# Kernel optimization log

Measured on AMD Instinct MI355X. Metric: run time of the kernel, lower is better.

## Reference

```python
import jax, jax.numpy as jnp
import numpy as np

N, E, H, NH = 50000, 800000, 128, 4
D = H // NH
EPS = 1e-5


def _ln(x, g, b):
    m = jnp.mean(x, axis=-1, keepdims=True)
    v = jnp.mean((x - m) ** 2, axis=-1, keepdims=True)
    return (x - m) * jax.lax.rsqrt(v + EPS) * g + b


def setup_inputs() -> dict:
    key = jax.random.key(0)
    ks = jax.random.split(key, 16)

    def lin(k, fi, fo):
        w = jax.random.normal(k, (fi, fo), jnp.float32) * (1.0 / np.sqrt(fi))
        return w, jnp.zeros((fo,), jnp.float32)

    h = jax.random.normal(ks[0], (N, H), jnp.float32)
    e = jax.random.normal(ks[1], (E, H), jnp.float32)
    src = jax.random.randint(ks[2], (E,), 0, N, jnp.int32)
    dst = jax.random.randint(ks[3], (E,), 0, N, jnp.int32)

    Wq, bq = lin(ks[4], H, H)
    Wk, bk = lin(ks[5], 2 * H, H)
    Wv, bv = lin(ks[6], 2 * H, H)
    Wn1, bn1 = lin(ks[7], H, H)
    Wn2, bn2 = lin(ks[8], H, H)
    We1, be1 = lin(ks[9], 3 * H, H)
    We2, be2 = lin(ks[10], H, H)
    gh = jnp.ones((H,), jnp.float32)
    bh = jnp.zeros((H,), jnp.float32)
    ge = jnp.ones((H,), jnp.float32)
    be = jnp.zeros((H,), jnp.float32)

    return dict(h=h, e=e, src=src, dst=dst, Wq=Wq, bq=bq, Wk=Wk, bk=bk,
                Wv=Wv, bv=bv, Wn1=Wn1, bn1=bn1, Wn2=Wn2, bn2=bn2,
                We1=We1, be1=be1, We2=We2, be2=be2, gh=gh, bh=bh, ge=ge, be=be)


def reference(h, e, src, dst, Wq, bq, Wk, bk, Wv, bv, Wn1, bn1, Wn2, bn2,
              We1, be1, We2, be2, gh, bh, ge, be):
    # gather src node features onto edges, concat with edge features: [E, 2H]
    m = jnp.concatenate([h[src], e], axis=-1)
    Q = (h @ Wq + bq).reshape(N, NH, D)
    K = (m @ Wk + bk).reshape(E, NH, D)
    V = (m @ Wv + bv).reshape(E, NH, D)

    # per-edge multihead attention score against destination query: [E, NH]
    s = jnp.sum(Q[dst] * K, axis=-1) / np.sqrt(D).astype(np.float32)

    # destination-grouped (segment) softmax per head
    smax = jax.ops.segment_max(s, dst, num_segments=N)  # [N, NH]
    a = jnp.exp(s - smax[dst])
    denom = jax.ops.segment_sum(a, dst, num_segments=N)  # [N, NH]
    a = a / denom[dst]

    # weighted scatter-sum of values back to destination nodes
    msg = V * a[..., None]  # [E, NH, D]
    h_agg = jax.ops.segment_sum(msg, dst, num_segments=N).reshape(N, H)

    # node MLP update (dropout = identity in eval) + residual + LayerNorm
    h_new = jax.nn.relu(jax.nn.relu(h_agg @ Wn1 + bn1) @ Wn2 + bn2)
    h_out = _ln(h + h_new, gh, bh)

    # edge MLP update on [src_h, dst_h, e] + residual + LayerNorm
    me = jnp.concatenate([h_out[src], h_out[dst], e], axis=-1)  # [E, 3H]
    e_new = jax.nn.relu(jax.nn.relu(me @ We1 + be1) @ We2 + be2)
    e_out = _ln(e + e_new, ge, be)
    return h_out, e_out
```

## Files before the change

### kernel.cpp

```cpp
#include <hip/hip_runtime.h>
#include <hip/hip_bf16.h>

#define NN 50000
#define EE 800000
#define HH 128

typedef __attribute__((ext_vector_type(8))) short bf16x8;
typedef __attribute__((ext_vector_type(4))) float f32x4;

__device__ inline unsigned short f2bf(float f) {
    union { float f; unsigned u; } v; v.f = f;
    unsigned r = v.u + 0x7FFF + ((v.u >> 16) & 1);
    return (unsigned short)(r >> 16);
}

__global__ __launch_bounds__(256) void hist_k(const int* __restrict__ dst, int* __restrict__ cnt) {
    int i = blockIdx.x * 256 + threadIdx.x;
    if (i < EE) atomicAdd(&cnt[dst[i]], 1);
}

__global__ __launch_bounds__(256) void blocksum_k(const int* __restrict__ cnt, int* __restrict__ bsum) {
    __shared__ int sm[256];
    int i = blockIdx.x * 256 + threadIdx.x;
    sm[threadIdx.x] = (i < NN) ? cnt[i] : 0;
    __syncthreads();
    for (int s = 128; s > 0; s >>= 1) {
        if (threadIdx.x < s) sm[threadIdx.x] += sm[threadIdx.x + s];
        __syncthreads();
    }
    if (threadIdx.x == 0) bsum[blockIdx.x] = sm[0];
}

__global__ __launch_bounds__(256) void scanb_k(int* __restrict__ bsum, int nb) {
    __shared__ int sm[256];
    int t = threadIdx.x;
    sm[t] = (t < nb) ? bsum[t] : 0;
    __syncthreads();
    for (int d = 1; d < 256; d <<= 1) {
        int v = (t >= d) ? sm[t - d] : 0;
        __syncthreads();
        sm[t] += v;
        __syncthreads();
    }
    if (t < nb) bsum[t] = sm[t];
}

__global__ __launch_bounds__(256) void offsets_k(const int* __restrict__ cnt, const int* __restrict__ bsum,
                                                 int* __restrict__ offsets, int* __restrict__ cursor) {
    __shared__ int sm[256];
    int b = blockIdx.x, t = threadIdx.x;
    int i = b * 256 + t;
    int c = (i < NN) ? cnt[i] : 0;
    sm[t] = c;
    __syncthreads();
    for (int d = 1; d < 256; d <<= 1) {
        int v = (t >= d) ? sm[t - d] : 0;
        __syncthreads();
        sm[t] += v;
        __syncthreads();
    }
    int incl = sm[t];
    int base = (b == 0) ? 0 : bsum[b - 1];
    int off = base + incl - c;
    if (i < NN) { offsets[i] = off; cursor[i] = off; }
    if (i == NN - 1) offsets[NN] = off + c;
}

__global__ __launch_bounds__(256) void fill_k(const int* __restrict__ src, const int* __restrict__ dst,
                                              int* __restrict__ cursor, int* __restrict__ eids,
                                              int* __restrict__ srcc, int* __restrict__ dstc) {
    int i = blockIdx.x * 256 + threadIdx.x;
    if (i < EE) {
        int d = dst[i];
        int p = atomicAdd(&cursor[d], 1);
        eids[p] = i;
        srcc[p] = src[i];
        dstc[p] = d;
    }
}

__global__ __launch_bounds__(256) void wprep_k(const float* __restrict__ W, unsigned short* __restrict__ out,
                                               int fi, int fo, int n_off, int out_ld) {
    int i = blockIdx.x * 256 + threadIdx.x;
    if (i >= fi * fo) return;
    int n = i / fi, k = i - n * fi;
    out[(size_t)(n_off + n) * out_ld + k] = f2bf(W[(size_t)k * fo + n]);
}

__global__ __launch_bounds__(256) void cvt_k(const float* __restrict__ in, unsigned short* __restrict__ out,
                                             long n8) {
    long i = (long)blockIdx.x * 256 + threadIdx.x;
    if (i >= n8) return;
    const float4* p = (const float4*)in + i * 2;
    float4 a = p[0], b = p[1];
    bf16x8 o = {(short)f2bf(a.x), (short)f2bf(a.y), (short)f2bf(a.z), (short)f2bf(a.w),
                (short)f2bf(b.x), (short)f2bf(b.y), (short)f2bf(b.z), (short)f2bf(b.w)};
    *((bf16x8*)out + i) = o;
}

__global__ __launch_bounds__(256) void cvtcsr_k(const float* __restrict__ e, const int* __restrict__ eids,
                                                unsigned short* __restrict__ out) {
    long gid = (long)blockIdx.x * 256 + threadIdx.x;
    long j = gid >> 4;
    if (j >= EE) return;
    int part = (int)(gid & 15);
    int rid = eids[j];
    const float4* p = (const float4*)(e + (size_t)rid * HH + part * 8);
    float4 a = p[0], b = p[1];
    bf16x8 o = {(short)f2bf(a.x), (short)f2bf(a.y), (short)f2bf(a.z), (short)f2bf(a.w),
                (short)f2bf(b.x), (short)f2bf(b.y), (short)f2bf(b.z), (short)f2bf(b.w)};
    *((bf16x8*)(out + (size_t)j * HH + part * 8)) = o;
}

template <int G, int NCW, int RT, int MODE>
__global__ __launch_bounds__(512, 2) void mm4_k(
    const unsigned short* __restrict__ A0, const int* __restrict__ idx0,
    const unsigned short* __restrict__ Wt, const float* __restrict__ bias,
    int M,
    float* __restrict__ Cf, unsigned short* __restrict__ Cb, int out_ld)
{
    constexpr int RW = 8 / NCW;
    constexpr int ROWS = RW * RT * 16;
    constexpr int Ktot = G * 128;
    constexpr int SI = ROWS / 32;
    __shared__ unsigned short Asl[G * ROWS * 128];

    const int t = threadIdx.x;
    const int wid = t >> 6, lane = t & 63;
    const int lr = lane & 15, lk = lane >> 4;
    const int colw = wid & 3;
    const int roww = wid >> 2;
    const int col0 = colw << 5;
    const int tbase = blockIdx.x * ROWS;

    #pragma unroll
    for (int g = 0; g < G; ++g) {
        #pragma unroll
        for (int i = 0; i < SI; ++i) {
            int rl = ((i * 8 + wid) << 2) + (lane >> 4);
            int gr = tbase + rl; if (gr >= M) gr = M - 1;
            int rid = idx0 ? idx0[gr] : gr;
            const unsigned short* src = A0 + (size_t)rid * HH + (((lane & 15) ^ (rl & 7)) << 3);
            unsigned short* dst = &Asl[(g * ROWS + ((i * 8 + wid) << 2)) << 7];
            __builtin_amdgcn_global_load_lds((const __attribute__((address_space(1))) void*)src,
                                             (__attribute__((address_space(3))) void*)dst, 16, 0, 0);
        }
    }

    f32x4 acc[RT][2];
    #pragma unroll
    for (int tt = 0; tt < RT; ++tt) { acc[tt][0] = (f32x4){0,0,0,0}; acc[tt][1] = (f32x4){0,0,0,0}; }

    __syncthreads();

    #pragma unroll
    for (int g = 0; g < G; ++g) {
        bf16x8 b[4][2];
        #pragma unroll
        for (int s = 0; s < 4; ++s)
            #pragma unroll
            for (int c = 0; c < 2; ++c)
                b[s][c] = *(const bf16x8*)(Wt + (size_t)(col0 + (c << 4) + lr) * Ktot + (g << 7) + (s << 5) + (lk << 3));

        #pragma unroll
        for (int tt = 0; tt < RT; ++tt) {
            const int tl = (tt * RW + roww) << 4;
            bf16x8 a[4];
            #pragma unroll
            for (int s = 0; s < 4; ++s) {
                const int c16 = ((s << 2) + lk) ^ (lr & 7);
                a[s] = *(const bf16x8*)&Asl[((g * ROWS + tl + lr) << 7) + (c16 << 3)];
            }
            #pragma unroll
            for (int s = 0; s < 4; ++s) {
                acc[tt][0] = __builtin_amdgcn_mfma_f32_16x16x32_bf16(a[s], b[s][0], acc[tt][0], 0, 0, 0);
                acc[tt][1] = __builtin_amdgcn_mfma_f32_16x16x32_bf16(a[s], b[s][1], acc[tt][1], 0, 0, 0);
            }
        }
    }

    float bias2[2] = {bias[col0 + lr], bias[col0 + 16 + lr]};
    #pragma unroll
    for (int tt = 0; tt < RT; ++tt) {
        #pragma unroll
        for (int rr = 0; rr < 4; ++rr) {
            int row = tbase + ((tt * RW + roww) << 4) + (lk << 2) + rr;
            if (row >= M) continue;
            #pragma unroll
            for (int c = 0; c < 2; ++c) {
                float v = acc[tt][c][rr] + bias2[c];
                if (MODE == 1) v = fmaxf(v, 0.f);
                size_t o = (size_t)row * out_ld + col0 + (c << 4) + lr;
                if (MODE == 0 || MODE == 1) Cf[o] = v;
                else Cb[o] = f2bf(v);
            }
        }
    }
}

template <int G, int RT>
__global__ __launch_bounds__(512, 2) void mlp_k(
    const unsigned short* __restrict__ A0, const int* __restrict__ idx0,
    const unsigned short* __restrict__ W1t, const float* __restrict__ b1,
    const unsigned short* __restrict__ W2t, const float* __restrict__ b2,
    int M,
    float* __restrict__ Cf, unsigned short* __restrict__ Cb2,
    const float* __restrict__ resid, const float* __restrict__ gamma, const float* __restrict__ beta)
{
    constexpr int RW = 2, NCW = 4;
    constexpr int ROWS = RW * RT * 16;
    constexpr int K1 = G * 128;
    constexpr int SI = ROWS / 32;
    __shared__ unsigned short Asl[G * ROWS * 128];
    __shared__ float lnbuf[RT * 32 * 8];

    const int t = threadIdx.x;
    const int wid = t >> 6, lane = t & 63;
    const int lr = lane & 15, lk = lane >> 4;
    const int colw = wid & 3, roww = wid >> 2;
    const int col0 = colw << 5;
    const int tbase = blockIdx.x * ROWS;

    #pragma unroll
    for (int g = 0; g < G; ++g) {
        #pragma unroll
        for (int i = 0; i < SI; ++i) {
            int rl = ((i * 8 + wid) << 2) + (lane >> 4);
            int gr = tbase + rl; if (gr >= M) gr = M - 1;
            int rid = idx0 ? idx0[gr] : gr;
            const unsigned short* src = A0 + (size_t)rid * HH + (((lane & 15) ^ (rl & 7)) << 3);
            unsigned short* dst = &Asl[(g * ROWS + ((i * 8 + wid) << 2)) << 7];
            __builtin_amdgcn_global_load_lds((const __attribute__((address_space(1))) void*)src,
                                             (__attribute__((address_space(3))) void*)dst, 16, 0, 0);
        }
    }

    f32x4 acc[RT][2];
    #pragma unroll
    for (int tt = 0; tt < RT; ++tt) { acc[tt][0] = (f32x4){0,0,0,0}; acc[tt][1] = (f32x4){0,0,0,0}; }

    __syncthreads();

    #pragma unroll
    for (int g = 0; g < G; ++g) {
        bf16x8 b[4][2];
        #pragma unroll
        for (int s = 0; s < 4; ++s)
            #pragma unroll
            for (int c = 0; c < 2; ++c)
                b[s][c] = *(const bf16x8*)(W1t + (size_t)(col0 + (c << 4) + lr) * K1 + (g << 7) + (s << 5) + (lk << 3));

        #pragma unroll
        for (int tt = 0; tt < RT; ++tt) {
            const int tl = (tt * RW + roww) << 4;
            bf16x8 a[4];
            #pragma unroll
            for (int s = 0; s < 4; ++s) {
                const int c16 = ((s << 2) + lk) ^ (lr & 7);
                a[s] = *(const bf16x8*)&Asl[((g * ROWS + tl + lr) << 7) + (c16 << 3)];
            }
            #pragma unroll
            for (int s = 0; s < 4; ++s) {
                acc[tt][0] = __builtin_amdgcn_mfma_f32_16x16x32_bf16(a[s], b[s][0], acc[tt][0], 0, 0, 0);
                acc[tt][1] = __builtin_amdgcn_mfma_f32_16x16x32_bf16(a[s], b[s][1], acc[tt][1], 0, 0, 0);
            }
        }
    }

    __syncthreads();

    {
        float b1c[2] = {b1[col0 + lr], b1[col0 + 16 + lr]};
        #pragma unroll
        for (int tt = 0; tt < RT; ++tt) {
            #pragma unroll
            for (int rr = 0; rr < 4; ++rr) {
                int rowl = ((tt * RW + roww) << 4) + (lk << 2) + rr;
                #pragma unroll
                for (int c = 0; c < 2; ++c) {
                    int col = col0 + (c << 4) + lr;
                    int chunk = (col >> 3) ^ (rowl & 7);
                    Asl[(rowl << 7) + (chunk << 3) + (col & 7)] =
                        f2bf(fmaxf(acc[tt][c][rr] + b1c[c], 0.f));
                }
            }
        }
    }

    __syncthreads();

    f32x4 acc2[RT][2];
    #pragma unroll
    for (int tt = 0; tt < RT; ++tt) { acc2[tt][0] = (f32x4){0,0,0,0}; acc2[tt][1] = (f32x4){0,0,0,0}; }

    {
        bf16x8 b[4][2];
        #pragma unroll
        for (int s = 0; s < 4; ++s)
            #pragma unroll
            for (int c = 0; c < 2; ++c)
                b[s][c] = *(const bf16x8*)(W2t + (size_t)(col0 + (c << 4) + lr) * 128 + (s << 5) + (lk << 3));

        #pragma unroll
        for (int tt = 0; tt < RT; ++tt) {
            const int tl = (tt * RW + roww) << 4;
            bf16x8 a[4];
            #pragma unroll
            for (int s = 0; s < 4; ++s) {
                const int c16 = ((s << 2) + lk) ^ (lr & 7);
                a[s] = *(const bf16x8*)&Asl[((tl + lr) << 7) + (c16 << 3)];
            }
            #pragma unroll
            for (int s = 0; s < 4; ++s) {
                acc2[tt][0] = __builtin_amdgcn_mfma_f32_16x16x32_bf16(a[s], b[s][0], acc2[tt][0], 0, 0, 0);
                acc2[tt][1] = __builtin_amdgcn_mfma_f32_16x16x32_bf16(a[s], b[s][1], acc2[tt][1], 0, 0, 0);
            }
        }
    }

    float b2c[2] = {b2[col0 + lr], b2[col0 + 16 + lr]};
    float g2[2] = {gamma[col0 + lr], gamma[col0 + 16 + lr]};
    float be2[2] = {beta[col0 + lr], beta[col0 + 16 + lr]};

    #pragma unroll
    for (int tt = 0; tt < RT; ++tt) {
        #pragma unroll
        for (int rr = 0; rr < 4; ++rr) {
            int row = tbase + ((tt * RW + roww) << 4) + (lk << 2) + rr;
            int rowc = (row < M) ? row : M - 1;
            float sum = 0.f, sq = 0.f;
            #pragma unroll
            for (int c = 0; c < 2; ++c) {
                float v = fmaxf(acc2[tt][c][rr] + b2c[c], 0.f);
                v += resid[(size_t)rowc * HH + col0 + (c << 4) + lr];
                acc2[tt][c][rr] = v;
                sum += v; sq += v * v;
            }
            sum += __shfl_xor(sum, 1); sq += __shfl_xor(sq, 1);
            sum += __shfl_xor(sum, 2); sq += __shfl_xor(sq, 2);
            sum += __shfl_xor(sum, 4); sq += __shfl_xor(sq, 4);
            sum += __shfl_xor(sum, 8); sq += __shfl_xor(sq, 8);
            if (lr == 0) {
                int rls = (roww << 4) + (lk << 2) + rr;
                lnbuf[((tt * 32 + rls) << 3) + (colw << 1) + 0] = sum;
                lnbuf[((tt * 32 + rls) << 3) + (colw << 1) + 1] = sq;
            }
        }
    }
    __syncthreads();
    #pragma unroll
    for (int tt = 0; tt < RT; ++tt) {
        #pragma unroll
        for (int rr = 0; rr < 4; ++rr) {
            int rls = (roww << 4) + (lk << 2) + rr;
            float s4 = 0.f, q4 = 0.f;
            #pragma unroll
            for (int cw = 0; cw < 4; ++cw) {
                s4 += lnbuf[((tt * 32 + rls) << 3) + (cw << 1) + 0];
                q4 += lnbuf[((tt * 32 + rls) << 3) + (cw << 1) + 1];
            }
            const float mean = s4 * (1.f / 128.f);
            const float var = q4 * (1.f / 128.f) - mean * mean;
            const float rs = rsqrtf(var + 1e-5f);
            int row = tbase + ((tt * RW + roww) << 4) + (lk << 2) + rr;
            if (row < M) {
                #pragma unroll
                for (int c = 0; c < 2; ++c) {
                    float o = (acc2[tt][c][rr] - mean) * rs * g2[c] + be2[c];
                    size_t idx = (size_t)row * HH + col0 + (c << 4) + lr;
                    Cf[idx] = o;
                    if (Cb2) Cb2[idx] = f2bf(o);
                }
            }
        }
    }
}

__global__ __launch_bounds__(512, 2) void mlpe_k(
    const unsigned short* __restrict__ ho, const int* __restrict__ src,
    const int* __restrict__ dst, const float* __restrict__ e,
    const unsigned short* __restrict__ W1t, const float* __restrict__ b1,
    const unsigned short* __restrict__ W2t, const float* __restrict__ b2,
    int M,
    float* __restrict__ Cf,
    const float* __restrict__ gamma, const float* __restrict__ beta)
{
    constexpr int RW = 2, RT = 2;
    constexpr int ROWS = RW * RT * 16;
    constexpr int K1 = 384;
    __shared__ unsigned short Asl[2 * ROWS * 128];
    __shared__ float Esl[ROWS * 128];
    __shared__ float lnbuf[RT * 32 * 8];

    const int t = threadIdx.x;
    const int wid = t >> 6, lane = t & 63;
    const int lr = lane & 15, lk = lane >> 4;
    const int colw = wid & 3, roww = wid >> 2;
    const int col0 = colw << 5;
    const int tbase = blockIdx.x * ROWS;

    #pragma unroll
    for (int g = 0; g < 2; ++g) {
        const int* ig = g ? dst : src;
        #pragma unroll
        for (int i = 0; i < 2; ++i) {
            int rl = ((i * 8 + wid) << 2) + (lane >> 4);
            int gr = tbase + rl; if (gr >= M) gr = M - 1;
            int rid = ig[gr];
            const unsigned short* sp = ho + (size_t)rid * HH + (((lane & 15) ^ (rl & 7)) << 3);
            unsigned short* dp = &Asl[(g * ROWS + ((i * 8 + wid) << 2)) << 7];
            __builtin_amdgcn_global_load_lds((const __attribute__((address_space(1))) void*)sp,
                                             (__attribute__((address_space(3))) void*)dp, 16, 0, 0);
        }
    }
    #pragma unroll
    for (int i = 0; i < 4; ++i) {
        int row = i * 16 + wid * 2 + (lane >> 5);
        int c16 = lane & 31;
        int c16s = (c16 & 24) | ((c16 & 7) ^ (row & 7));
        int gr = tbase + row; if (gr >= M) gr = M - 1;
        const float* sp = e + (size_t)gr * HH + c16s * 4;
        float* dp = &Esl[(i * 16 + wid * 2) * 128 + (lane >> 5) * 128];
        dp = &Esl[(i * 512 + wid * 64) * 4 / 4] + 0;
        float* dbase = Esl + (size_t)(i * 512 + wid * 64) * 4;
        (void)dp;
        __builtin_amdgcn_global_load_lds((const __attribute__((address_space(1))) void*)sp,
                                         (__attribute__((address_space(3))) void*)dbase, 16, 0, 0);
    }

    f32x4 acc[RT][2];
    #pragma unroll
    for (int tt = 0; tt < RT; ++tt) { acc[tt][0] = (f32x4){0,0,0,0}; acc[tt][1] = (f32x4){0,0,0,0}; }

    __syncthreads();

    #pragma unroll
    for (int g = 0; g < 3; ++g) {
        bf16x8 b[4][2];
        #pragma unroll
        for (int s = 0; s < 4; ++s)
            #pragma unroll
            for (int c = 0; c < 2; ++c)
                b[s][c] = *(const bf16x8*)(W1t + (size_t)(col0 + (c << 4) + lr) * K1 + (g << 7) + (s << 5) + (lk << 3));

        #pragma unroll
        for (int tt = 0; tt < RT; ++tt) {
            const int tl = (tt * RW + roww) << 4;
            const int r = tl + lr;
            bf16x8 a[4];
            if (g < 2) {
                #pragma unroll
                for (int s = 0; s < 4; ++s) {
                    const int c16 = ((s << 2) + lk) ^ (lr & 7);
                    a[s] = *(const bf16x8*)&Asl[((g * ROWS + r) << 7) + (c16 << 3)];
                }
            } else {
                #pragma unroll
                for (int s = 0; s < 4; ++s) {
                    int c16a = (s << 3) + (lk << 1);
                    int c16b = c16a + 1;
                    int ca = (c16a & 24) | ((c16a & 7) ^ (r & 7));
                    int cb = (c16b & 24) | ((c16b & 7) ^ (r & 7));
                    float4 fa = *(const float4*)&Esl[r * 128 + ca * 4];
                    float4 fb = *(const float4*)&Esl[r * 128 + cb * 4];
                    a[s] = (bf16x8){(short)f2bf(fa.x), (short)f2bf(fa.y), (short)f2bf(fa.z), (short)f2bf(fa.w),
                                    (short)f2bf(fb.x), (short)f2bf(fb.y), (short)f2bf(fb.z), (short)f2bf(fb.w)};
                }
            }
            #pragma unroll
            for (int s = 0; s < 4; ++s) {
                acc[tt][0] = __builtin_amdgcn_mfma_f32_16x16x32_bf16(a[s], b[s][0], acc[tt][0], 0, 0, 0);
                acc[tt][1] = __builtin_amdgcn_mfma_f32_16x16x32_bf16(a[s], b[s][1], acc[tt][1], 0, 0, 0);
            }
        }
    }

    __syncthreads();

    {
        float b1c[2] = {b1[col0 + lr], b1[col0 + 16 + lr]};
        #pragma unroll
        for (int tt = 0; tt < RT; ++tt) {
            #pragma unroll
            for (int rr = 0; rr < 4; ++rr) {
                int rowl = ((tt * RW + roww) << 4) + (lk << 2) + rr;
                #pragma unroll
                for (int c = 0; c < 2; ++c) {
                    int col = col0 + (c << 4) + lr;
                    int chunk = (col >> 3) ^ (rowl & 7);
                    Asl[(rowl << 7) + (chunk << 3) + (col & 7)] =
                        f2bf(fmaxf(acc[tt][c][rr] + b1c[c], 0.f));
                }
            }
        }
    }

    __syncthreads();

    f32x4 acc2[RT][2];
    #pragma unroll
    for (int tt = 0; tt < RT; ++tt) { acc2[tt][0] = (f32x4){0,0,0,0}; acc2[tt][1] = (f32x4){0,0,0,0}; }

    {
        bf16x8 b[4][2];
        #pragma unroll
        for (int s = 0; s < 4; ++s)
            #pragma unroll
            for (int c = 0; c < 2; ++c)
                b[s][c] = *(const bf16x8*)(W2t + (size_t)(col0 + (c << 4) + lr) * 128 + (s << 5) + (lk << 3));

        #pragma unroll
        for (int tt = 0; tt < RT; ++tt) {
            const int tl = (tt * RW + roww) << 4;
            bf16x8 a[4];
            #pragma unroll
            for (int s = 0; s < 4; ++s) {
                const int c16 = ((s << 2) + lk) ^ (lr & 7);
                a[s] = *(const bf16x8*)&Asl[((tl + lr) << 7) + (c16 << 3)];
            }
            #pragma unroll
            for (int s = 0; s < 4; ++s) {
                acc2[tt][0] = __builtin_amdgcn_mfma_f32_16x16x32_bf16(a[s], b[s][0], acc2[tt][0], 0, 0, 0);
                acc2[tt][1] = __builtin_amdgcn_mfma_f32_16x16x32_bf16(a[s], b[s][1], acc2[tt][1], 0, 0, 0);
            }
        }
    }

    float b2c[2] = {b2[col0 + lr], b2[col0 + 16 + lr]};
    float g2[2] = {gamma[col0 + lr], gamma[col0 + 16 + lr]};
    float be2[2] = {beta[col0 + lr], beta[col0 + 16 + lr]};

    #pragma unroll
    for (int tt = 0; tt < RT; ++tt) {
        #pragma unroll
        for (int rr = 0; rr < 4; ++rr) {
            int rowl = ((tt * RW + roww) << 4) + (lk << 2) + rr;
            float sum = 0.f, sq = 0.f;
            #pragma unroll
            for (int c = 0; c < 2; ++c) {
                int col = col0 + (c << 4) + lr;
                int c16 = col >> 2;
                int cs = (c16 & 24) | ((c16 & 7) ^ (rowl & 7));
                float rv = Esl[rowl * 128 + cs * 4 + (col & 3)];
                float v = fmaxf(acc2[tt][c][rr] + b2c[c], 0.f) + rv;
                acc2[tt][c][rr] = v;
                sum += v; sq += v * v;
            }
            sum += __shfl_xor(sum, 1); sq += __shfl_xor(sq, 1);
            sum += __shfl_xor(sum, 2); sq += __shfl_xor(sq, 2);
            sum += __shfl_xor(sum, 4); sq += __shfl_xor(sq, 4);
            sum += __shfl_xor(sum, 8); sq += __shfl_xor(sq, 8);
            if (lr == 0) {
                int rls = (roww << 4) + (lk << 2) + rr;
                lnbuf[((tt * 32 + rls) << 3) + (colw << 1) + 0] = sum;
                lnbuf[((tt * 32 + rls) << 3) + (colw << 1) + 1] = sq;
            }
        }
    }
    __syncthreads();
    #pragma unroll
    for (int tt = 0; tt < RT; ++tt) {
        #pragma unroll
        for (int rr = 0; rr < 4; ++rr) {
            int rls = (roww << 4) + (lk << 2) + rr;
            float s4 = 0.f, q4 = 0.f;
            #pragma unroll
            for (int cw = 0; cw < 4; ++cw) {
                s4 += lnbuf[((tt * 32 + rls) << 3) + (cw << 1) + 0];
                q4 += lnbuf[((tt * 32 + rls) << 3) + (cw << 1) + 1];
            }
            const float mean = s4 * (1.f / 128.f);
            const float var = q4 * (1.f / 128.f) - mean * mean;
            const float rs = rsqrtf(var + 1e-5f);
            int row = tbase + ((tt * RW + roww) << 4) + (lk << 2) + rr;
            if (row < M) {
                #pragma unroll
                for (int c = 0; c < 2; ++c)
                    Cf[(size_t)row * HH + col0 + (c << 4) + lr] =
                        (acc2[tt][c][rr] - mean) * rs * g2[c] + be2[c];
            }
        }
    }
}

template <int RT>
__global__ __launch_bounds__(512, 2) void kv_k(
    const unsigned short* __restrict__ hbf, const int* __restrict__ srcc,
    const unsigned short* __restrict__ ebfc,
    const unsigned short* __restrict__ Wt, const float* __restrict__ bias,
    const float* __restrict__ Q, const int* __restrict__ dstc,
    int M, unsigned short* __restrict__ V, float* __restrict__ sbuf)
{
    constexpr int ROWS = RT * 16;
    constexpr int Ktot = 256;
    constexpr int SI = ROWS / 32;
    __shared__ unsigned short Asl[2 * ROWS * 128];

    const int t = threadIdx.x;
    const int wid = t >> 6, lane = t & 63;
    const int lr = lane & 15, lk = lane >> 4;
    const int col0 = wid << 5;
    const int tbase = blockIdx.x * ROWS;

    int dstid[RT][4];
    if (wid < 4) {
        #pragma unroll
        for (int tt = 0; tt < RT; ++tt)
            #pragma unroll
            for (int rr = 0; rr < 4; ++rr) {
                int row = tbase + (tt << 4) + (lk << 2) + rr;
                dstid[tt][rr] = dstc[(row < M) ? row : M - 1];
            }
    }

    #pragma unroll
    for (int g = 0; g < 2; ++g) {
        const unsigned short* Ag = g ? ebfc : hbf;
        #pragma unroll
        for (int i = 0; i < SI; ++i) {
            int rl = ((i * 8 + wid) << 2) + (lane >> 4);
            int gr = tbase + rl; if (gr >= M) gr = M - 1;
            int rid = g ? gr : srcc[gr];
            const unsigned short* srcp = Ag + (size_t)rid * HH + (((lane & 15) ^ (rl & 7)) << 3);
            unsigned short* dstp = &Asl[(g * ROWS + ((i * 8 + wid) << 2)) << 7];
            __builtin_amdgcn_global_load_lds((const __attribute__((address_space(1))) void*)srcp,
                                             (__attribute__((address_space(3))) void*)dstp, 16, 0, 0);
        }
    }

    f32x4 acc[RT][2];
    #pragma unroll
    for (int tt = 0; tt < RT; ++tt) { acc[tt][0] = (f32x4){0,0,0,0}; acc[tt][1] = (f32x4){0,0,0,0}; }

    __syncthreads();

    #pragma unroll
    for (int g = 0; g < 2; ++g) {
        bf16x8 b[4][2];
        #pragma unroll
        for (int s = 0; s < 4; ++s)
            #pragma unroll
            for (int c = 0; c < 2; ++c)
                b[s][c] = *(const bf16x8*)(Wt + (size_t)(col0 + (c << 4) + lr) * Ktot + (g << 7) + (s << 5) + (lk << 3));

        #pragma unroll
        for (int tt = 0; tt < RT; ++tt) {
            bf16x8 a[4];
            #pragma unroll
            for (int s = 0; s < 4; ++s) {
                const int c16 = ((s << 2) + lk) ^ (lr & 7);
                a[s] = *(const bf16x8*)&Asl[((g * ROWS + (tt << 4) + lr) << 7) + (c16 << 3)];
            }
            #pragma unroll
            for (int s = 0; s < 4; ++s) {
                acc[tt][0] = __builtin_amdgcn_mfma_f32_16x16x32_bf16(a[s], b[s][0], acc[tt][0], 0, 0, 0);
                acc[tt][1] = __builtin_amdgcn_mfma_f32_16x16x32_bf16(a[s], b[s][1], acc[tt][1], 0, 0, 0);
            }
        }
    }

    float bias2[2] = {bias[col0 + lr], bias[col0 + 16 + lr]};

    if (wid < 4) {
        #pragma unroll
        for (int tt = 0; tt < RT; ++tt) {
            #pragma unroll
            for (int rr = 0; rr < 4; ++rr) {
                int row = tbase + (tt << 4) + (lk << 2) + rr;
                int d = dstid[tt][rr];
                float q0 = Q[(size_t)d * HH + col0 + lr];
                float q1 = Q[(size_t)d * HH + col0 + 16 + lr];
                float p = (acc[tt][0][rr] + bias2[0]) * q0 + (acc[tt][1][rr] + bias2[1]) * q1;
                p += __shfl_xor(p, 1); p += __shfl_xor(p, 2);
                p += __shfl_xor(p, 4); p += __shfl_xor(p, 8);
                if (lr == 0 && row < M)
                    sbuf[(size_t)row * 4 + wid] = p * 0.17677669529663687f;
            }
        }
    } else {
        #pragma unroll
        for (int tt = 0; tt < RT; ++tt) {
            #pragma unroll
            for (int rr = 0; rr < 4; ++rr) {
                int row = tbase + (tt << 4) + (lk << 2) + rr;
                if (row >= M) continue;
                #pragma unroll
                for (int c = 0; c < 2; ++c)
                    V[(size_t)row * HH + (col0 - 128) + (c << 4) + lr] = f2bf(acc[tt][c][rr] + bias2[c]);
            }
        }
    }
}

__global__ __launch_bounds__(256) void agg_k(const __hip_bfloat16* __restrict__ Vb,
                                             const float* __restrict__ s,
                                             const int* __restrict__ offsets,
                                             unsigned short* __restrict__ hagg)
{
    const int t = threadIdx.x;
    const int n = blockIdx.x * 4 + (t >> 6);
    if (n >= NN) return;
    const int lane = t & 63;
    const int c0 = lane, c1 = lane + 64;
    const int h0 = lane >> 5, h1 = h0 + 2;
    const int o0 = offsets[n], o1 = offsets[n + 1];
    float m0 = -1e30f, m1 = -1e30f, d0 = 0.f, d1 = 0.f, a0 = 0.f, a1 = 0.f;
    for (int j = o0; j < o1; ++j) {
        const float s0 = s[(size_t)j * 4 + h0];
        const float s1 = s[(size_t)j * 4 + h1];
        const float v0 = __bfloat162float(Vb[(size_t)j * HH + c0]);
        const float v1 = __bfloat162float(Vb[(size_t)j * HH + c1]);
        float nm = fmaxf(m0, s0);
        float sc = __expf(m0 - nm);
        float w  = __expf(s0 - nm);
        d0 = d0 * sc + w; a0 = a0 * sc + w * v0; m0 = nm;
        nm = fmaxf(m1, s1);
        sc = __expf(m1 - nm);
        w  = __expf(s1 - nm);
        d1 = d1 * sc + w; a1 = a1 * sc + w * v1; m1 = nm;
    }
    const bool any = (o1 > o0);
    hagg[(size_t)n * HH + c0] = any ? f2bf(a0 / d0) : 0;
    hagg[(size_t)n * HH + c1] = any ? f2bf(a1 / d1) : 0;
}

extern "C" void kernel_launch(void* const* d_in, const int* in_sizes, int n_in,
                              void* d_out, int out_size, void* d_ws, size_t ws_size,
                              hipStream_t stream)
{
    const float* h   = (const float*)d_in[0];
    const float* e   = (const float*)d_in[1];
    const int*   src = (const int*)d_in[2];
    const int*   dst = (const int*)d_in[3];
    const float* Wq  = (const float*)d_in[4];
    const float* bq  = (const float*)d_in[5];
    const float* Wk  = (const float*)d_in[6];
    const float* bk  = (const float*)d_in[7];
    const float* Wv  = (const float*)d_in[8];
    const float* bv  = (const float*)d_in[9];
    const float* Wn1 = (const float*)d_in[10];
    const float* bn1 = (const float*)d_in[11];
    const float* Wn2 = (const float*)d_in[12];
    const float* bn2 = (const float*)d_in[13];
    const float* We1 = (const float*)d_in[14];
    const float* be1 = (const float*)d_in[15];
    const float* We2 = (const float*)d_in[16];
    const float* be2 = (const float*)d_in[17];
    const float* gh  = (const float*)d_in[18];
    const float* bh  = (const float*)d_in[19];
    const float* ge  = (const float*)d_in[20];
    const float* be_ = (const float*)d_in[21];
    (void)in_sizes; (void)n_in; (void)out_size; (void)ws_size;

    float* h_out = (float*)d_out;
    float* e_out = (float*)d_out + (size_t)NN * HH;

    char* ws = (char*)d_ws;
    size_t off = 0;
    auto carve = [&](size_t bytes) { void* p = ws + off; off += (bytes + 255) & ~(size_t)255; return p; };
    unsigned short* Vbuf = (unsigned short*)carve((size_t)EE * HH * 2);
    unsigned short* ebfc = (unsigned short*)carve((size_t)EE * HH * 2);
    float* Q      = (float*)carve((size_t)NN * HH * 4);
    float* sbuf   = (float*)carve((size_t)EE * 4 * 4);
    unsigned short* hagg = (unsigned short*)carve((size_t)NN * HH * 2);
    unsigned short* hobf = (unsigned short*)carve((size_t)NN * HH * 2);
    unsigned short* hbf  = (unsigned short*)carve((size_t)NN * HH * 2);
    int* cursor   = (int*)carve((size_t)NN * 4);
    int* offsets  = (int*)carve((size_t)(NN + 1) * 4);
    int* bsum     = (int*)carve(256 * 4);
    int* eids     = (int*)carve((size_t)EE * 4);
    int* srcc     = (int*)carve((size_t)EE * 4);
    int* dstc     = (int*)carve((size_t)EE * 4);
    unsigned short* Wq_s  = (unsigned short*)carve(128 * 128 * 2);
    unsigned short* Wkv_s = (unsigned short*)carve(256 * 256 * 2);
    unsigned short* Wn1_s = (unsigned short*)carve(128 * 128 * 2);
    unsigned short* Wn2_s = (unsigned short*)carve(128 * 128 * 2);
    unsigned short* We1_s = (unsigned short*)carve(128 * 384 * 2);
    unsigned short* We2_s = (unsigned short*)carve(128 * 128 * 2);
    float* b_kv   = (float*)carve(256 * 4);

    const int nb = (NN + 255) / 256;

    wprep_k<<<(128 * 128 + 255) / 256, 256, 0, stream>>>(Wq,  Wq_s,  128, 128, 0, 128);
    wprep_k<<<(256 * 128 + 255) / 256, 256, 0, stream>>>(Wk,  Wkv_s, 256, 128, 0, 256);
    wprep_k<<<(256 * 128 + 255) / 256, 256, 0, stream>>>(Wv,  Wkv_s, 256, 128, 128, 256);
    wprep_k<<<(128 * 128 + 255) / 256, 256, 0, stream>>>(Wn1, Wn1_s, 128, 128, 0, 128);
    wprep_k<<<(128 * 128 + 255) / 256, 256, 0, stream>>>(Wn2, Wn2_s, 128, 128, 0, 128);
    wprep_k<<<(384 * 128 + 255) / 256, 256, 0, stream>>>(We1, We1_s, 384, 128, 0, 384);
    wprep_k<<<(128 * 128 + 255) / 256, 256, 0, stream>>>(We2, We2_s, 128, 128, 0, 128);
    hipMemcpyAsync(b_kv,       bk, 128 * 4, hipMemcpyDeviceToDevice, stream);
    hipMemcpyAsync(b_kv + 128, bv, 128 * 4, hipMemcpyDeviceToDevice, stream);

    cvt_k<<<(NN * HH / 8 + 255) / 256, 256, 0, stream>>>(h, hbf, (long)NN * HH / 8);

    hipMemsetAsync(cursor, 0, (size_t)NN * 4, stream);
    hist_k<<<(EE + 255) / 256, 256, 0, stream>>>(dst, cursor);
    blocksum_k<<<nb, 256, 0, stream>>>(cursor, bsum);
    scanb_k<<<1, 256, 0, stream>>>(bsum, nb);
    offsets_k<<<nb, 256, 0, stream>>>(cursor, bsum, offsets, cursor);
    fill_k<<<(EE + 255) / 256, 256, 0, stream>>>(src, dst, cursor, eids, srcc, dstc);

    cvtcsr_k<<<(EE * 16 + 255) / 256, 256, 0, stream>>>(e, eids, ebfc);

    mm4_k<1, 4, 4, 0><<<(NN + 127) / 128, 512, 0, stream>>>(
        hbf, nullptr, Wq_s, bq, NN, Q, nullptr, 128);

    kv_k<4><<<EE / 64, 512, 0, stream>>>(
        hbf, srcc, ebfc, Wkv_s, b_kv, Q, dstc, EE, Vbuf, sbuf);

    agg_k<<<(NN + 3) / 4, 256, 0, stream>>>((const __hip_bfloat16*)Vbuf, sbuf, offsets, hagg);

    mlp_k<1, 4><<<(NN + 127) / 128, 512, 0, stream>>>(
        hagg, nullptr, Wn1_s, bn1, Wn2_s, bn2, NN, h_out, hobf, h, gh, bh);

    mlpe_k<<<EE / 64, 512, 0, stream>>>(
        hobf, src, dst, e, We1_s, be1, We2_s, be2, EE, e_out, ge, be_);
}
```

Baseline: 1.246 ms.

## Make edge GEMM kernels persistent with double-buffered LDS staging

Both per-edge kernels (K/V projection with score, and the edge MLP with LayerNorm) become persistent: 500 blocks each loop over many tiles, with the next tile's gathered inputs loaded asynchronously into a second LDS buffer while the current tile is computed. The edge MLP tile shrinks to 32 rows, uses a separate buffer for the hidden activations, and uses a lighter LDS-only barrier between its stages. The aim is to hide gather latency and cut per-block launch and prologue overhead. In exchange LDS use per block grows, the grid is fixed at 500 blocks, which may leave CUs underused or unbalanced, and weights are still reloaded every tile.

```diff
diff --git a/kernel.cpp b/kernel.cpp
--- a/kernel.cpp
+++ b/kernel.cpp
@@ -12,6 +12,12 @@
     union { float f; unsigned u; } v; v.f = f;
     unsigned r = v.u + 0x7FFF + ((v.u >> 16) & 1);
     return (unsigned short)(r >> 16);
+}
+
+__device__ __forceinline__ void lds_barrier() {
+    asm volatile("s_waitcnt lgkmcnt(0)" ::: "memory");
+    __builtin_amdgcn_sched_barrier(0);
+    __builtin_amdgcn_s_barrier();
 }
 
 __global__ __launch_bounds__(256) void hist_k(const int* __restrict__ dst, int* __restrict__ cnt) {
@@ -376,7 +382,125 @@
     }
 }
 
-__global__ __launch_bounds__(512, 2) void mlpe_k(
+template <int TPB>
+__global__ __launch_bounds__(512, 2) void kvt_k(
+    const unsigned short* __restrict__ hbf, const int* __restrict__ srcc,
+    const unsigned short* __restrict__ ebfc,
+    const unsigned short* __restrict__ Wt, const float* __restrict__ bias,
+    const float* __restrict__ Q, const int* __restrict__ dstc,
+    int M, unsigned short* __restrict__ V, float* __restrict__ sbuf)
+{
+    __shared__ unsigned short Abuf[2][2 * 64 * 128];
+
+    const int t = threadIdx.x;
+    const int wid = t >> 6, lane = t & 63;
+    const int lr = lane & 15, lk = lane >> 4;
+    const int col0 = wid << 5;
+    const int tb = blockIdx.x * TPB;
+
+    auto stage = [&](int tile, int buf) {
+        const int base = tile * 64;
+        #pragma unroll
+        for (int g = 0; g < 2; ++g) {
+            const unsigned short* Ag = g ? ebfc : hbf;
+            #pragma unroll
+            for (int i = 0; i < 2; ++i) {
+                int rl = ((i * 8 + wid) << 2) + (lane >> 4);
+                int gr = base + rl; if (gr >= M) gr = M - 1;
+                int rid = g ? gr : srcc[gr];
+                const unsigned short* sp = Ag + (size_t)rid * HH + (((lane & 15) ^ (rl & 7)) << 3);
+                unsigned short* dp = &Abuf[buf][(g * 64 + ((i * 8 + wid) << 2)) << 7];
+                __builtin_amdgcn_global_load_lds((const __attribute__((address_space(1))) void*)sp,
+                                                 (__attribute__((address_space(3))) void*)dp, 16, 0, 0);
+            }
+        }
+    };
+
+    float bias2[2] = {bias[col0 + lr], bias[col0 + 16 + lr]};
+
+    stage(tb, 0);
+
+    for (int tt = 0; tt < TPB; ++tt) {
+        const int cur = tt & 1;
+        const int rbase = (tb + tt) * 64;
+
+        __syncthreads();
+        if (tt + 1 < TPB) stage(tb + tt + 1, cur ^ 1);
+
+        int dstid[4][4];
+        if (wid < 4) {
+            #pragma unroll
+            for (int t4 = 0; t4 < 4; ++t4)
+                #pragma unroll
+                for (int rr = 0; rr < 4; ++rr) {
+                    int row = rbase + (t4 << 4) + (lk << 2) + rr;
+                    dstid[t4][rr] = dstc[(row < M) ? row : M - 1];
+                }
+        }
+
+        f32x4 acc[4][2];
+        #pragma unroll
+        for (int t4 = 0; t4 < 4; ++t4) { acc[t4][0] = (f32x4){0,0,0,0}; acc[t4][1] = (f32x4){0,0,0,0}; }
+
+        #pragma unroll
+        for (int g = 0; g < 2; ++g) {
+            bf16x8 b[4][2];
+            #pragma unroll
+            for (int s = 0; s < 4; ++s)
+                #pragma unroll
+                for (int c = 0; c < 2; ++c)
+                    b[s][c] = *(const bf16x8*)(Wt + (size_t)(col0 + (c << 4) + lr) * 256 + (g << 7) + (s << 5) + (lk << 3));
+
+            #pragma unroll
+            for (int t4 = 0; t4 < 4; ++t4) {
+                bf16x8 a[4];
+                #pragma unroll
+                for (int s = 0; s < 4; ++s) {
+                    const int c16 = ((s << 2) + lk) ^ (lr & 7);
+                    a[s] = *(const bf16x8*)&Abuf[cur][((g * 64 + (t4 << 4) + lr) << 7) + (c16 << 3)];
+                }
+                #pragma unroll
+                for (int s = 0; s < 4; ++s) {
+                    acc[t4][0] = __builtin_amdgcn_mfma_f32_16x16x32_bf16(a[s], b[s][0], acc[t4][0], 0, 0, 0);
+                    acc[t4][1] = __builtin_amdgcn_mfma_f32_16x16x32_bf16(a[s], b[s][1], acc[t4][1], 0, 0, 0);
+                }
+            }
+        }
+
+        if (wid < 4) {
+            #pragma unroll
+            for (int t4 = 0; t4 < 4; ++t4) {
+                #pragma unroll
+                for (int rr = 0; rr < 4; ++rr) {
+                    int row = rbase + (t4 << 4) + (lk << 2) + rr;
+                    int d = dstid[t4][rr];
+                    float q0 = Q[(size_t)d * HH + col0 + lr];
+                    float q1 = Q[(size_t)d * HH + col0 + 16 + lr];
+                    float p = (acc[t4][0][rr] + bias2[0]) * q0 + (acc[t4][1][rr] + bias2[1]) * q1;
+                    p += __shfl_xor(p, 1); p += __shfl_xor(p, 2);
+                    p += __shfl_xor(p, 4); p += __shfl_xor(p, 8);
+                    if (lr == 0 && row < M)
+                        sbuf[(size_t)row * 4 + wid] = p * 0.17677669529663687f;
+                }
+            }
+        } else {
+            #pragma unroll
+            for (int t4 = 0; t4 < 4; ++t4) {
+                #pragma unroll
+                for (int rr = 0; rr < 4; ++rr) {
+                    int row = rbase + (t4 << 4) + (lk << 2) + rr;
+                    if (row >= M) continue;
+                    #pragma unroll
+                    for (int c = 0; c < 2; ++c)
+                        V[(size_t)row * HH + (col0 - 128) + (c << 4) + lr] = f2bf(acc[t4][c][rr] + bias2[c]);
+                }
+            }
+        }
+    }
+}
+
+template <int TPB>
+__global__ __launch_bounds__(512, 2) void mlpet_k(
     const unsigned short* __restrict__ ho, const int* __restrict__ src,
     const int* __restrict__ dst, const float* __restrict__ e,
     const unsigned short* __restrict__ W1t, const float* __restrict__ b1,
@@ -385,74 +509,74 @@
     float* __restrict__ Cf,
     const float* __restrict__ gamma, const float* __restrict__ beta)
 {
-    constexpr int RW = 2, RT = 2;
-    constexpr int ROWS = RW * RT * 16;
-    constexpr int K1 = 384;
-    __shared__ unsigned short Asl[2 * ROWS * 128];
-    __shared__ float Esl[ROWS * 128];
-    __shared__ float lnbuf[RT * 32 * 8];
+    __shared__ unsigned short Abuf[2][2 * 32 * 128];
+    __shared__ float Ebuf[2][32 * 128];
+    __shared__ unsigned short tbuf[32 * 128];
+    __shared__ float lnbuf[32 * 8];
 
     const int t = threadIdx.x;
     const int wid = t >> 6, lane = t & 63;
     const int lr = lane & 15, lk = lane >> 4;
-    const int colw = wid & 3, roww = wid >> 2;
+    const int colw = wid & 3, rg = wid >> 2;
     const int col0 = colw << 5;
-    const int tbase = blockIdx.x * ROWS;
-
-    #pragma unroll
-    for (int g = 0; g < 2; ++g) {
-        const int* ig = g ? dst : src;
-        #pragma unroll
-        for (int i = 0; i < 2; ++i) {
-            int rl = ((i * 8 + wid) << 2) + (lane >> 4);
-            int gr = tbase + rl; if (gr >= M) gr = M - 1;
+    const int tb = blockIdx.x * TPB;
+
+    auto stage = [&](int tile, int buf) {
+        const int base = tile * 32;
+        #pragma unroll
+        for (int g = 0; g < 2; ++g) {
+            const int* ig = g ? dst : src;
+            int rl = t >> 4;
+            int gr = base + rl; if (gr >= M) gr = M - 1;
             int rid = ig[gr];
-            const unsigned short* sp = ho + (size_t)rid * HH + (((lane & 15) ^ (rl & 7)) << 3);
-            unsigned short* dp = &Asl[(g * ROWS + ((i * 8 + wid) << 2)) << 7];
+            const unsigned short* sp = ho + (size_t)rid * HH + (((t & 15) ^ (rl & 7)) << 3);
+            unsigned short* dp = &Abuf[buf][((g * 32) << 7) + (wid << 9)];
             __builtin_amdgcn_global_load_lds((const __attribute__((address_space(1))) void*)sp,
                                              (__attribute__((address_space(3))) void*)dp, 16, 0, 0);
         }
-    }
-    #pragma unroll
-    for (int i = 0; i < 4; ++i) {
-        int row = i * 16 + wid * 2 + (lane >> 5);
-        int c16 = lane & 31;
-        int c16s = (c16 & 24) | ((c16 & 7) ^ (row & 7));
-        int gr = tbase + row; if (gr >= M) gr = M - 1;
-        const float* sp = e + (size_t)gr * HH + c16s * 4;
-        float* dp = &Esl[(i * 16 + wid * 2) * 128 + (lane >> 5) * 128];
-        dp = &Esl[(i * 512 + wid * 64) * 4 / 4] + 0;
-        float* dbase = Esl + (size_t)(i * 512 + wid * 64) * 4;
-        (void)dp;
-        __builtin_amdgcn_global_load_lds((const __attribute__((address_space(1))) void*)sp,
-                                         (__attribute__((address_space(3))) void*)dbase, 16, 0, 0);
-    }
-
-    f32x4 acc[RT][2];
-    #pragma unroll
-    for (int tt = 0; tt < RT; ++tt) { acc[tt][0] = (f32x4){0,0,0,0}; acc[tt][1] = (f32x4){0,0,0,0}; }
-
-    __syncthreads();
-
-    #pragma unroll
-    for (int g = 0; g < 3; ++g) {
-        bf16x8 b[4][2];
-        #pragma unroll
-        for (int s = 0; s < 4; ++s)
-            #pragma unroll
-            for (int c = 0; c < 2; ++c)
-                b[s][c] = *(const bf16x8*)(W1t + (size_t)(col0 + (c << 4) + lr) * K1 + (g << 7) + (s << 5) + (lk << 3));
-
-        #pragma unroll
-        for (int tt = 0; tt < RT; ++tt) {
-            const int tl = (tt * RW + roww) << 4;
-            const int r = tl + lr;
+        #pragma unroll
+        for (int i = 0; i < 2; ++i) {
+            int row = i * 16 + (t >> 5);
+            int c16 = t & 31;
+            int c16s = (c16 & 24) | ((c16 & 7) ^ (row & 7));
+            int gr = base + row; if (gr >= M) gr = M - 1;
+            const float* sp = e + (size_t)gr * HH + c16s * 4;
+            float* dp = Ebuf[buf] + i * 2048 + wid * 256;
+            __builtin_amdgcn_global_load_lds((const __attribute__((address_space(1))) void*)sp,
+                                             (__attribute__((address_space(3))) void*)dp, 16, 0, 0);
+        }
+    };
+
+    float b1c[2] = {b1[col0 + lr], b1[col0 + 16 + lr]};
+    float b2c[2] = {b2[col0 + lr], b2[col0 + 16 + lr]};
+    float g2[2]  = {gamma[col0 + lr], gamma[col0 + 16 + lr]};
+    float be2[2] = {beta[col0 + lr], beta[col0 + 16 + lr]};
+
+    stage(tb, 0);
+
+    for (int tt = 0; tt < TPB; ++tt) {
+        const int cur = tt & 1;
+        const int rbase = (tb + tt) * 32;
+
+        __syncthreads();
+        if (tt + 1 < TPB) stage(tb + tt + 1, cur ^ 1);
+
+        f32x4 acc[2] = {(f32x4){0,0,0,0}, (f32x4){0,0,0,0}};
+        const int r = rg * 16 + lr;
+        #pragma unroll
+        for (int g = 0; g < 3; ++g) {
+            bf16x8 b[4][2];
+            #pragma unroll
+            for (int s = 0; s < 4; ++s)
+                #pragma unroll
+                for (int c = 0; c < 2; ++c)
+                    b[s][c] = *(const bf16x8*)(W1t + (size_t)(col0 + (c << 4) + lr) * 384 + (g << 7) + (s << 5) + (lk << 3));
             bf16x8 a[4];
             if (g < 2) {
                 #pragma unroll
                 for (int s = 0; s < 4; ++s) {
                     const int c16 = ((s << 2) + lk) ^ (lr & 7);
-                    a[s] = *(const bf16x8*)&Asl[((g * ROWS + r) << 7) + (c16 << 3)];
+                    a[s] = *(const bf16x8*)&Abuf[cur][((g * 32 + r) << 7) + (c16 << 3)];
                 }
             } else {
                 #pragma unroll
@@ -461,89 +585,66 @@
                     int c16b = c16a + 1;
                     int ca = (c16a & 24) | ((c16a & 7) ^ (r & 7));
                     int cb = (c16b & 24) | ((c16b & 7) ^ (r & 7));
-                    float4 fa = *(const float4*)&Esl[r * 128 + ca * 4];
-                    float4 fb = *(const float4*)&Esl[r * 128 + cb * 4];
+                    float4 fa = *(const float4*)&Ebuf[cur][r * 128 + ca * 4];
+                    float4 fb = *(const float4*)&Ebuf[cur][r * 128 + cb * 4];
                     a[s] = (bf16x8){(short)f2bf(fa.x), (short)f2bf(fa.y), (short)f2bf(fa.z), (short)f2bf(fa.w),
                                     (short)f2bf(fb.x), (short)f2bf(fb.y), (short)f2bf(fb.z), (short)f2bf(fb.w)};
                 }
             }
             #pragma unroll
             for (int s = 0; s < 4; ++s) {
-                acc[tt][0] = __builtin_amdgcn_mfma_f32_16x16x32_bf16(a[s], b[s][0], acc[tt][0], 0, 0, 0);
-                acc[tt][1] = __builtin_amdgcn_mfma_f32_16x16x32_bf16(a[s], b[s][1], acc[tt][1], 0, 0, 0);
-            }
-        }
-    }
-
-    __syncthreads();
-
-    {
-        float b1c[2] = {b1[col0 + lr], b1[col0 + 16 + lr]};
-        #pragma unroll
-        for (int tt = 0; tt < RT; ++tt) {
-            #pragma unroll
-            for (int rr = 0; rr < 4; ++rr) {
-                int rowl = ((tt * RW + roww) << 4) + (lk << 2) + rr;
-                #pragma unroll
-                for (int c = 0; c < 2; ++c) {
-                    int col = col0 + (c << 4) + lr;
-                    int chunk = (col >> 3) ^ (rowl & 7);
-                    Asl[(rowl << 7) + (chunk << 3) + (col & 7)] =
-                        f2bf(fmaxf(acc[tt][c][rr] + b1c[c], 0.f));
-                }
-            }
-        }
-    }
-
-    __syncthreads();
-
-    f32x4 acc2[RT][2];
-    #pragma unroll
-    for (int tt = 0; tt < RT; ++tt) { acc2[tt][0] = (f32x4){0,0,0,0}; acc2[tt][1] = (f32x4){0,0,0,0}; }
-
-    {
-        bf16x8 b[4][2];
-        #pragma unroll
-        for (int s = 0; s < 4; ++s)
-            #pragma unroll
-            for (int c = 0; c < 2; ++c)
-                b[s][c] = *(const bf16x8*)(W2t + (size_t)(col0 + (c << 4) + lr) * 128 + (s << 5) + (lk << 3));
-
-        #pragma unroll
-        for (int tt = 0; tt < RT; ++tt) {
-            const int tl = (tt * RW + roww) << 4;
+                acc[0] = __builtin_amdgcn_mfma_f32_16x16x32_bf16(a[s], b[s][0], acc[0], 0, 0, 0);
+                acc[1] = __builtin_amdgcn_mfma_f32_16x16x32_bf16(a[s], b[s][1], acc[1], 0, 0, 0);
+            }
+        }
+
+        #pragma unroll
+        for (int rr = 0; rr < 4; ++rr) {
+            int rowl = rg * 16 + (lk << 2) + rr;
+            #pragma unroll
+            for (int c = 0; c < 2; ++c) {
+                int col = col0 + (c << 4) + lr;
+                int chunk = (col >> 3) ^ (rowl & 7);
+                tbuf[(rowl << 7) + (chunk << 3) + (col & 7)] =
+                    f2bf(fmaxf(acc[c][rr] + b1c[c], 0.f));
+            }
+        }
+        lds_barrier();
+
+        f32x4 acc2[2] = {(f32x4){0,0,0,0}, (f32x4){0,0,0,0}};
+        {
+            bf16x8 b[4][2];
+            #pragma unroll
+            for (int s = 0; s < 4; ++s)
+                #pragma unroll
+                for (int c = 0; c < 2; ++c)
+                    b[s][c] = *(const bf16x8*)(W2t + (size_t)(col0 + (c << 4) + lr) * 128 + (s << 5) + (lk << 3));
             bf16x8 a[4];
             #pragma unroll
             for (int s = 0; s < 4; ++s) {
                 const int c16 = ((s << 2) + lk) ^ (lr & 7);
-                a[s] = *(const bf16x8*)&Asl[((tl + lr) << 7) + (c16 << 3)];
+                a[s] = *(const bf16x8*)&tbuf[(r << 7) + (c16 << 3)];
             }
             #pragma unroll
             for (int s = 0; s < 4; ++s) {
-                acc2[tt][0] = __builtin_amdgcn_mfma_f32_16x16x32_bf16(a[s], b[s][0], acc2[tt][0], 0, 0, 0);
-                acc2[tt][1] = __builtin_amdgcn_mfma_f32_16x16x32_bf16(a[s], b[s][1], acc2[tt][1], 0, 0, 0);
-            }
-        }
-    }
-
-    float b2c[2] = {b2[col0 + lr], b2[col0 + 16 + lr]};
-    float g2[2] = {gamma[col0 + lr], gamma[col0 + 16 + lr]};
-    float be2[2] = {beta[col0 + lr], beta[col0 + 16 + lr]};
-
-    #pragma unroll
-    for (int tt = 0; tt < RT; ++tt) {
+                acc2[0] = __builtin_amdgcn_mfma_f32_16x16x32_bf16(a[s], b[s][0], acc2[0], 0, 0, 0);
+                acc2[1] = __builtin_amdgcn_mfma_f32_16x16x32_bf16(a[s], b[s][1], acc2[1], 0, 0, 0);
+            }
+        }
+
+        float xv[4][2];
         #pragma unroll
         for (int rr = 0; rr < 4; ++rr) {
-            int rowl = ((tt * RW + roww) << 4) + (lk << 2) + rr;
+            int rowl = rg * 16 + (lk << 2) + rr;
             float sum = 0.f, sq = 0.f;
             #pragma unroll
             for (int c = 0; c < 2; ++c) {
                 int col = col0 + (c << 4) + lr;
                 int c16 = col >> 2;
                 int cs = (c16 & 24) | ((c16 & 7) ^ (rowl & 7));
-                float rv = Esl[rowl * 128 + cs * 4 + (col & 3)];
-                float v = fmaxf(acc2[tt][c][rr] + b2c[c], 0.f) + rv;
-                acc2[tt][c][rr] = v;
+                float rv = Ebuf[cur][rowl * 128 + cs * 4 + (col & 3)];
+                float v = fmaxf(acc2[c][rr] + b2c[c], 0.f) + rv;
+                xv[rr][c] = v;
                 sum += v; sq += v * v;
             }
             sum += __shfl_xor(sum, 1); sq += __shfl_xor(sq, 1);
@@ -551,142 +652,30 @@
             sum += __shfl_xor(sum, 4); sq += __shfl_xor(sq, 4);
             sum += __shfl_xor(sum, 8); sq += __shfl_xor(sq, 8);
             if (lr == 0) {
-                int rls = (roww << 4) + (lk << 2) + rr;
-                lnbuf[((tt * 32 + rls) << 3) + (colw << 1) + 0] = sum;
-                lnbuf[((tt * 32 + rls) << 3) + (colw << 1) + 1] = sq;
-            }
-        }
-    }
-    __syncthreads();
-    #pragma unroll
-    for (int tt = 0; tt < RT; ++tt) {
+                lnbuf[(rowl << 3) + (colw << 1) + 0] = sum;
+                lnbuf[(rowl << 3) + (colw << 1) + 1] = sq;
+            }
+        }
+        lds_barrier();
+
         #pragma unroll
         for (int rr = 0; rr < 4; ++rr) {
-            int rls = (roww << 4) + (lk << 2) + rr;
+            int rowl = rg * 16 + (lk << 2) + rr;
             float s4 = 0.f, q4 = 0.f;
             #pragma unroll
             for (int cw = 0; cw < 4; ++cw) {
-                s4 += lnbuf[((tt * 32 + rls) << 3) + (cw << 1) + 0];
-                q4 += lnbuf[((tt * 32 + rls) << 3) + (cw << 1) + 1];
+                s4 += lnbuf[(rowl << 3) + (cw << 1) + 0];
+                q4 += lnbuf[(rowl << 3) + (cw << 1) + 1];
             }
             const float mean = s4 * (1.f / 128.f);
             const float var = q4 * (1.f / 128.f) - mean * mean;
             const float rs = rsqrtf(var + 1e-5f);
-            int row = tbase + ((tt * RW + roww) << 4) + (lk << 2) + rr;
+            int row = rbase + rowl;
             if (row < M) {
                 #pragma unroll
                 for (int c = 0; c < 2; ++c)
                     Cf[(size_t)row * HH + col0 + (c << 4) + lr] =
-                        (acc2[tt][c][rr] - mean) * rs * g2[c] + be2[c];
-            }
-        }
-    }
-}
-
-template <int RT>
-__global__ __launch_bounds__(512, 2) void kv_k(
-    const unsigned short* __restrict__ hbf, const int* __restrict__ srcc,
-    const unsigned short* __restrict__ ebfc,
-    const unsigned short* __restrict__ Wt, const float* __restrict__ bias,
-    const float* __restrict__ Q, const int* __restrict__ dstc,
-    int M, unsigned short* __restrict__ V, float* __restrict__ sbuf)
-{
-    constexpr int ROWS = RT * 16;
-    constexpr int Ktot = 256;
-    constexpr int SI = ROWS / 32;
-    __shared__ unsigned short Asl[2 * ROWS * 128];
-
-    const int t = threadIdx.x;
-    const int wid = t >> 6, lane = t & 63;
-    const int lr = lane & 15, lk = lane >> 4;
-    const int col0 = wid << 5;
-    const int tbase = blockIdx.x * ROWS;
-
-    int dstid[RT][4];
-    if (wid < 4) {
-        #pragma unroll
-        for (int tt = 0; tt < RT; ++tt)
-            #pragma unroll
-            for (int rr = 0; rr < 4; ++rr) {
-                int row = tbase + (tt << 4) + (lk << 2) + rr;
-                dstid[tt][rr] = dstc[(row < M) ? row : M - 1];
-            }
-    }
-
-    #pragma unroll
-    for (int g = 0; g < 2; ++g) {
-        const unsigned short* Ag = g ? ebfc : hbf;
-        #pragma unroll
-        for (int i = 0; i < SI; ++i) {
-            int rl = ((i * 8 + wid) << 2) + (lane >> 4);
-            int gr = tbase + rl; if (gr >= M) gr = M - 1;
-            int rid = g ? gr : srcc[gr];
-            const unsigned short* srcp = Ag + (size_t)rid * HH + (((lane & 15) ^ (rl & 7)) << 3);
-            unsigned short* dstp = &Asl[(g * ROWS + ((i * 8 + wid) << 2)) << 7];
-            __builtin_amdgcn_global_load_lds((const __attribute__((address_space(1))) void*)srcp,
-                                             (__attribute__((address_space(3))) void*)dstp, 16, 0, 0);
-        }
-    }
-
-    f32x4 acc[RT][2];
-    #pragma unroll
-    for (int tt = 0; tt < RT; ++tt) { acc[tt][0] = (f32x4){0,0,0,0}; acc[tt][1] = (f32x4){0,0,0,0}; }
-
-    __syncthreads();
-
-    #pragma unroll
-    for (int g = 0; g < 2; ++g) {
-        bf16x8 b[4][2];
-        #pragma unroll
-        for (int s = 0; s < 4; ++s)
-            #pragma unroll
-            for (int c = 0; c < 2; ++c)
-                b[s][c] = *(const bf16x8*)(Wt + (size_t)(col0 + (c << 4) + lr) * Ktot + (g << 7) + (s << 5) + (lk << 3));
-
-        #pragma unroll
-        for (int tt = 0; tt < RT; ++tt) {
-            bf16x8 a[4];
-            #pragma unroll
-            for (int s = 0; s < 4; ++s) {
-                const int c16 = ((s << 2) + lk) ^ (lr & 7);
-                a[s] = *(const bf16x8*)&Asl[((g * ROWS + (tt << 4) + lr) << 7) + (c16 << 3)];
-            }
-            #pragma unroll
-            for (int s = 0; s < 4; ++s) {
-                acc[tt][0] = __builtin_amdgcn_mfma_f32_16x16x32_bf16(a[s], b[s][0], acc[tt][0], 0, 0, 0);
-                acc[tt][1] = __builtin_amdgcn_mfma_f32_16x16x32_bf16(a[s], b[s][1], acc[tt][1], 0, 0, 0);
-            }
-        }
-    }
-
-    float bias2[2] = {bias[col0 + lr], bias[col0 + 16 + lr]};
-
-    if (wid < 4) {
-        #pragma unroll
-        for (int tt = 0; tt < RT; ++tt) {
-            #pragma unroll
-            for (int rr = 0; rr < 4; ++rr) {
-                int row = tbase + (tt << 4) + (lk << 2) + rr;
-                int d = dstid[tt][rr];
-                float q0 = Q[(size_t)d * HH + col0 + lr];
-                float q1 = Q[(size_t)d * HH + col0 + 16 + lr];
-                float p = (acc[tt][0][rr] + bias2[0]) * q0 + (acc[tt][1][rr] + bias2[1]) * q1;
-                p += __shfl_xor(p, 1); p += __shfl_xor(p, 2);
-                p += __shfl_xor(p, 4); p += __shfl_xor(p, 8);
-                if (lr == 0 && row < M)
-                    sbuf[(size_t)row * 4 + wid] = p * 0.17677669529663687f;
-            }
-        }
-    } else {
-        #pragma unroll
-        for (int tt = 0; tt < RT; ++tt) {
-            #pragma unroll
-            for (int rr = 0; rr < 4; ++rr) {
-                int row = tbase + (tt << 4) + (lk << 2) + rr;
-                if (row >= M) continue;
-                #pragma unroll
-                for (int c = 0; c < 2; ++c)
-                    V[(size_t)row * HH + (col0 - 128) + (c << 4) + lr] = f2bf(acc[tt][c][rr] + bias2[c]);
+                        (xv[rr][c] - mean) * rs * g2[c] + be2[c];
             }
         }
     }
@@ -805,7 +794,7 @@
     mm4_k<1, 4, 4, 0><<<(NN + 127) / 128, 512, 0, stream>>>(
         hbf, nullptr, Wq_s, bq, NN, Q, nullptr, 128);
 
-    kv_k<4><<<EE / 64, 512, 0, stream>>>(
+    kvt_k<25><<<500, 512, 0, stream>>>(
         hbf, srcc, ebfc, Wkv_s, b_kv, Q, dstc, EE, Vbuf, sbuf);
 
     agg_k<<<(NN + 3) / 4, 256, 0, stream>>>((const __hip_bfloat16*)Vbuf, sbuf, offsets, hagg);
@@ -813,6 +802,6 @@
     mlp_k<1, 4><<<(NN + 127) / 128, 512, 0, stream>>>(
         hagg, nullptr, Wn1_s, bn1, Wn2_s, bn2, NN, h_out, hobf, h, gh, bh);
 
-    mlpe_k<<<EE / 64, 512, 0, stream>>>(
+    mlpet_k<50><<<500, 512, 0, stream>>>(
         hobf, src, dst, e, We1_s, be1, We2_s, be2, EE, e_out, ge, be_);
 }
```

Measured after the change: 1.333 ms. +7.0%, slower.
